# Performance work log

Measured on AMD Instinct MI355X. Metric: run time of the kernel, lower is better.

## Reference

```python
import jax, jax.numpy as jnp
import numpy as np

GRID_SIZE = 5
SPLINE_ORDER = 3
GRID_RANGE = (-0.2, 0.2)
N_TOK, IN_CH, OUT_CH = 8192, 1024, 1024
K_COEF = GRID_SIZE + SPLINE_ORDER  # 8 basis functions per feature


def _make_grid():
    lo, hi = GRID_RANGE
    h = (hi - lo) / GRID_SIZE
    # 12 knots, extended by spline_order on both sides
    return (jnp.arange(-SPLINE_ORDER, GRID_SIZE + SPLINE_ORDER + 1, dtype=jnp.float32) * h + lo)


def _b_splines(x, grid):
    # x: [N, in] -> bases: [N, in, K_COEF] via Cox-de Boor recursion
    xe = x[..., None]                      # [N, in, 1]
    G = grid.shape[0]                      # 12
    bases = ((xe >= grid[:-1]) & (xe < grid[1:])).astype(x.dtype)  # [N, in, G-1]
    for k in range(1, SPLINE_ORDER + 1):
        left = (xe - grid[: G - k - 1]) / (grid[k : G - 1] - grid[: G - k - 1]) * bases[..., :-1]
        right = (grid[k + 1 :] - xe) / (grid[k + 1 :] - grid[1 : G - k]) * bases[..., 1:]
        bases = left + right
    return bases                            # [N, in, 8]


def _kan_layer(x, base_w, spline_w, grid):
    # base_activation = Identity
    base_out = x @ base_w.T                               # [N, out]
    bases = _b_splines(x, grid)                           # [N, in, K]
    spline_out = jnp.einsum('nik,oik->no', bases, spline_w)
    return base_out + spline_out


def setup_inputs() -> dict:
    key = jax.random.key(0)
    k1, k2, k3, k4, k5 = jax.random.split(key, 5)
    lo, hi = GRID_RANGE
    x = jax.random.uniform(k1, (N_TOK, IN_CH), dtype=jnp.float32, minval=lo, maxval=hi)
    s = 0.1 / np.sqrt(IN_CH)
    return {
        'x': x,
        'base_w1': jax.random.normal(k2, (OUT_CH, IN_CH), dtype=jnp.float32) * s,
        'spline_w1': jax.random.normal(k3, (OUT_CH, IN_CH, K_COEF), dtype=jnp.float32) * s,
        'base_w2': jax.random.normal(k4, (OUT_CH, OUT_CH), dtype=jnp.float32) * s,
        'spline_w2': jax.random.normal(k5, (OUT_CH, OUT_CH, K_COEF), dtype=jnp.float32) * s,
    }


def reference(x, base_w1, spline_w1, base_w2, spline_w2):
    grid = _make_grid()
    x1 = _kan_layer(x, base_w1, spline_w1, grid)
    x2 = _kan_layer(x1, base_w2, spline_w2, grid)
    return x2
```

## Files before the change

### kernel.cpp

```cpp
#include <hip/hip_runtime.h>
#include <hip/hip_bf16.h>

typedef __attribute__((ext_vector_type(8))) short bf16x8;
typedef __attribute__((ext_vector_type(4))) float f32x4;
typedef __attribute__((ext_vector_type(4))) unsigned int u32x4;

#define KCAT 9216
#define NTOK 8192
#define CH   1024
#define KHALF 4608
#define NT32 144

__device__ __forceinline__ unsigned short f2bf(float f) {
    union { float f; unsigned int u; } v; v.f = f;
    unsigned int r = v.u + 0x7fffu + ((v.u >> 16) & 1u);
    return (unsigned short)(r >> 16);
}

__device__ __forceinline__ void load16_to_lds(const void* gp, void* lp) {
    __builtin_amdgcn_global_load_lds(
        (__attribute__((address_space(1))) void*)(void*)gp,
        (__attribute__((address_space(3))) void*)lp,
        16, 0, 0);
}

__device__ __forceinline__ void bases8_cf(float x, unsigned int* w) {
    float p  = (x + 0.44f) * 12.5f;
    float mf = floorf(p);
    float u  = p - mf;
    int   m  = (int)mf;
    float v  = 1.0f - u;
    float u2 = u * u, u3 = u2 * u;
    float N0 = v * v * v * (1.0f / 6.0f);
    float N1 = 0.5f * u3 - u2 + (2.0f / 3.0f);
    float N3 = u3 * (1.0f / 6.0f);
    float N2 = 1.0f - N0 - N1 - N3;
    unsigned long long lo =
          (unsigned long long)f2bf(N0)
        | ((unsigned long long)f2bf(N1) << 16)
        | ((unsigned long long)f2bf(N2) << 32)
        | ((unsigned long long)f2bf(N3) << 48);
    lo = (m >= 0 && m <= 10) ? lo : 0ull;
    int sh  = (m - 3) * 16;
    int sh1 = sh - 64;
    unsigned long long d0 =
        (sh  >= 0) ? ((sh  < 64) ? (lo << sh)    : 0ull)
                   : ((-sh  < 64) ? (lo >> (-sh))  : 0ull);
    unsigned long long d1 =
        (sh1 >= 0) ? ((sh1 < 64) ? (lo << sh1)   : 0ull)
                   : ((-sh1 < 64) ? (lo >> (-sh1)) : 0ull);
    w[0] = (unsigned int)d0; w[1] = (unsigned int)(d0 >> 32);
    w[2] = (unsigned int)d1; w[3] = (unsigned int)(d1 >> 32);
}

__device__ __forceinline__ void conv_w_body(const float* __restrict__ BW,
                                            const float* __restrict__ SW,
                                            unsigned short* __restrict__ W, int o) {
    const float* bw = BW + (size_t)o * 1024;
    const float* sw = SW + (size_t)o * 8192;
    unsigned short* w = W + (size_t)o * KCAT;
    for (int c = threadIdx.x * 4; c < KCAT; c += 256 * 4) {
        const float* src = (c < 1024) ? (bw + c) : (sw + (c - 1024));
        float4 v = *(const float4*)src;
        unsigned short u[4] = { f2bf(v.x), f2bf(v.y), f2bf(v.z), f2bf(v.w) };
        *(unsigned long long*)(w + c) = *(unsigned long long*)u;
    }
}

__device__ __forceinline__ void basis_body(float x, unsigned short* __restrict__ A, int idx) {
    int n = idx >> 10, i = idx & 1023;
    size_t rowbase = (size_t)n * KCAT;
    A[rowbase + i] = f2bf(x);
    unsigned int w[4];
    bases8_cf(x, w);
    *(u32x4*)(A + rowbase + 1024 + (size_t)i * 8) = (u32x4){w[0], w[1], w[2], w[3]};
}

__global__ __launch_bounds__(256) void prep1(const float* __restrict__ BW1,
                                             const float* __restrict__ SW1,
                                             unsigned short* __restrict__ W,
                                             const float* __restrict__ X,
                                             unsigned short* __restrict__ A) {
    int b = blockIdx.x;
    if (b < 1024) { conv_w_body(BW1, SW1, W, b); return; }
    int bb = b - 1024;
    for (int idx = bb * 256 + threadIdx.x; idx < NTOK * CH; idx += 2048 * 256)
        basis_body(X[idx], A, idx);
}

__global__ __launch_bounds__(256) void mid2(const float* __restrict__ BW2,
                                            const float* __restrict__ SW2,
                                            unsigned short* __restrict__ W,
                                            const float* __restrict__ C0,
                                            const float* __restrict__ C1,
                                            unsigned short* __restrict__ A) {
    int b = blockIdx.x;
    if (b < 1024) { conv_w_body(BW2, SW2, W, b); return; }
    int bb = b - 1024;
    for (int idx = bb * 256 + threadIdx.x; idx < NTOK * CH; idx += 2048 * 256)
        basis_body(C0[idx] + C1[idx], A, idx);
}

__global__ __launch_bounds__(256) void add_out(const float* __restrict__ C0,
                                               const float* __restrict__ C1,
                                               float* __restrict__ out, int total4) {
    for (int i = blockIdx.x * 256 + threadIdx.x; i < total4; i += gridDim.x * 256) {
        float4 a = ((const float4*)C0)[i];
        float4 b = ((const float4*)C1)[i];
        float4 r = { a.x + b.x, a.y + b.y, a.z + b.z, a.w + b.w };
        ((float4*)out)[i] = r;
    }
}

__global__ __launch_bounds__(512, 2) void gemm256_splitk(const unsigned short* __restrict__ A,
                                                         const unsigned short* __restrict__ B,
                                                         float* __restrict__ C0,
                                                         float* __restrict__ C1) {
    __shared__ __align__(16) unsigned short As[4 * 256 * 32];
    __shared__ __align__(16) unsigned short Bs[4 * 256 * 32];
    const int tid  = threadIdx.x;
    const int lane = tid & 63;
    const int wid  = tid >> 6;
    const int wr = wid >> 2, wc = wid & 3;
    const int ln = lane & 15, q = lane >> 4;

    const int bid = blockIdx.x;
    const int xcd = bid & 7, ii = bid >> 3;
    const int kz = xcd & 1, chm = xcd >> 1;
    const int bm = chm * 8 + (ii & 7);
    const int bn = ii >> 3;

    const unsigned short* Ab = A + (size_t)(bm * 256) * KCAT + (size_t)kz * KHALF;
    const unsigned short* Bb = B + (size_t)(bn * 256) * KCAT + (size_t)kz * KHALF;
    float* C = (kz == 0) ? C0 : C1;

    f32x4 acc[8][4] = {};

    auto stage = [&](int tile, int ds) {
#pragma unroll
        for (int part = 0; part < 2; ++part) {
            int c = part * 512 + tid;
            int r = c >> 2;
            int gslot = (c & 3) ^ ((r >> 1) & 3);
            size_t goff = (size_t)r * (KCAT * 2) + (size_t)tile * 64 + gslot * 16;
            load16_to_lds((const char*)Ab + goff, (char*)As + (size_t)ds * 16384 + c * 16);
            load16_to_lds((const char*)Bb + goff, (char*)Bs + (size_t)ds * 16384 + c * 16);
        }
    };

    stage(0, 0);
    stage(1, 1);
    asm volatile("s_waitcnt vmcnt(4)" ::: "memory");
    __builtin_amdgcn_s_barrier();

    for (int g = 0; g < NT32 / 4; ++g) {
#pragma unroll
        for (int u = 0; u < 4; ++u) {
            const int tile = g * 4 + u;
            const bool pf = (tile + 2) < NT32;
            if (pf) stage(tile + 2, (u + 2) & 3);

            const char* Ah = (const char*)As + u * 16384;
            const char* Bh = (const char*)Bs + u * 16384;
            bf16x8 afr[8], bfr[4];
#pragma unroll
            for (int f = 0; f < 8; ++f) {
                int row = wr * 128 + f * 16 + ln;
                afr[f] = *(const bf16x8*)(Ah + row * 64 + ((q ^ ((row >> 1) & 3)) * 16));
            }
#pragma unroll
            for (int nf = 0; nf < 4; ++nf) {
                int row = wc * 64 + nf * 16 + ln;
                bfr[nf] = *(const bf16x8*)(Bh + row * 64 + ((q ^ ((row >> 1) & 3)) * 16));
            }
            __builtin_amdgcn_s_setprio(1);
#pragma unroll
            for (int f = 0; f < 8; ++f)
#pragma unroll
                for (int nf = 0; nf < 4; ++nf)
                    acc[f][nf] = __builtin_amdgcn_mfma_f32_16x16x32_bf16(
                        afr[f], bfr[nf], acc[f][nf], 0, 0, 0);
            __builtin_amdgcn_s_setprio(0);
            if (pf) asm volatile("s_waitcnt vmcnt(4)" ::: "memory");
            else    asm volatile("s_waitcnt vmcnt(0)" ::: "memory");
            __builtin_amdgcn_s_barrier();
        }
    }

#pragma unroll
    for (int mf = 0; mf < 8; ++mf)
#pragma unroll
        for (int nf = 0; nf < 4; ++nf)
#pragma unroll
            for (int r = 0; r < 4; ++r) {
                int row = bm * 256 + wr * 128 + mf * 16 + q * 4 + r;
                int col = bn * 256 + wc * 64 + nf * 16 + ln;
                C[(size_t)row * CH + col] = acc[mf][nf][r];
            }
}

extern "C" void kernel_launch(void* const* d_in, const int* in_sizes, int n_in,
                              void* d_out, int out_size, void* d_ws, size_t ws_size,
                              hipStream_t stream) {
    const float* x   = (const float*)d_in[0];
    const float* bw1 = (const float*)d_in[1];
    const float* sw1 = (const float*)d_in[2];
    const float* bw2 = (const float*)d_in[3];
    const float* sw2 = (const float*)d_in[4];
    float* out = (float*)d_out;

    char* ws = (char*)d_ws;
    unsigned short* Abuf = (unsigned short*)ws;
    unsigned short* Wbuf = (unsigned short*)(ws + 150994944);
    float* C0 = (float*)(ws + 150994944 + 18874368);
    float* C1 = (float*)(ws + 150994944 + 18874368 + 33554432);

    prep1         <<<dim3(3072), dim3(256), 0, stream>>>(bw1, sw1, Wbuf, x, Abuf);
    gemm256_splitk<<<dim3(256), dim3(512), 0, stream>>>(Abuf, Wbuf, C0, C1);

    mid2          <<<dim3(3072), dim3(256), 0, stream>>>(bw2, sw2, Wbuf, C0, C1, Abuf);
    gemm256_splitk<<<dim3(256), dim3(512), 0, stream>>>(Abuf, Wbuf, C0, C1);
    add_out       <<<dim3(1024), dim3(256), 0, stream>>>(C0, C1, out, NTOK * CH / 4);
}
```

Measured before the change: 488.8 us.

## Switch to 32x32x16 MFMA and load B fragments directly into registers

Replaces the 16x16x32 bf16 MFMA tiling with 32x32x16 instructions. It removes the LDS staging of the B operand, so each wave loads its B fragments straight from global memory into double-buffered registers, one tile ahead of use. The goal is to cut LDS traffic and halve shared memory use while keeping the A tile in the existing four-stage LDS pipeline. The trade-off is uncoalesced, wave-duplicated global loads of B (four waves share each column slice), more register pressure, and a hand-unrolled tail with adjusted vmcnt waits.

```diff
diff --git a/kernel.cpp b/kernel.cpp
--- a/kernel.cpp
+++ b/kernel.cpp
@@ -2,7 +2,7 @@
 #include <hip/hip_bf16.h>
 
 typedef __attribute__((ext_vector_type(8))) short bf16x8;
-typedef __attribute__((ext_vector_type(4))) float f32x4;
+typedef __attribute__((ext_vector_type(16))) float f32x16;
 typedef __attribute__((ext_vector_type(4))) unsigned int u32x4;
 
 #define KCAT 9216
@@ -117,12 +117,11 @@
                                                          float* __restrict__ C0,
                                                          float* __restrict__ C1) {
     __shared__ __align__(16) unsigned short As[4 * 256 * 32];
-    __shared__ __align__(16) unsigned short Bs[4 * 256 * 32];
     const int tid  = threadIdx.x;
     const int lane = tid & 63;
     const int wid  = tid >> 6;
     const int wr = wid >> 2, wc = wid & 3;
-    const int ln = lane & 15, q = lane >> 4;
+    const int l31 = lane & 31, h = lane >> 5;
 
     const int bid = blockIdx.x;
     const int xcd = bid & 7, ii = bid >> 3;
@@ -131,12 +130,14 @@
     const int bn = ii >> 3;
 
     const unsigned short* Ab = A + (size_t)(bm * 256) * KCAT + (size_t)kz * KHALF;
-    const unsigned short* Bb = B + (size_t)(bn * 256) * KCAT + (size_t)kz * KHALF;
+    const unsigned short* Bl = B + (size_t)(bn * 256 + wc * 64 + l31) * KCAT
+                                 + (size_t)kz * KHALF + (size_t)h * 8;
     float* C = (kz == 0) ? C0 : C1;
 
-    f32x4 acc[8][4] = {};
-
-    auto stage = [&](int tile, int ds) {
+    f32x16 acc[4][2] = {};
+    bf16x8 b0[2][2], b1[2][2];
+
+    auto stageA = [&](int tile, int ds) {
 #pragma unroll
         for (int part = 0; part < 2; ++part) {
             int c = part * 512 + tid;
@@ -144,57 +145,72 @@
             int gslot = (c & 3) ^ ((r >> 1) & 3);
             size_t goff = (size_t)r * (KCAT * 2) + (size_t)tile * 64 + gslot * 16;
             load16_to_lds((const char*)Ab + goff, (char*)As + (size_t)ds * 16384 + c * 16);
-            load16_to_lds((const char*)Bb + goff, (char*)Bs + (size_t)ds * 16384 + c * 16);
         }
     };
-
-    stage(0, 0);
-    stage(1, 1);
-    asm volatile("s_waitcnt vmcnt(4)" ::: "memory");
+    auto loadB = [&](bf16x8 (&dst)[2][2], int tile) {
+#pragma unroll
+        for (int nf = 0; nf < 2; ++nf)
+#pragma unroll
+            for (int ks = 0; ks < 2; ++ks)
+                dst[nf][ks] = *(const bf16x8*)(Bl + (size_t)nf * 32 * KCAT
+                                                  + (size_t)tile * 32 + ks * 16);
+    };
+    auto compute = [&](const bf16x8 (&bfr)[2][2], int u) {
+        const char* Ah = (const char*)As + u * 16384;
+        bf16x8 afr[8];
+#pragma unroll
+        for (int mf = 0; mf < 4; ++mf)
+#pragma unroll
+            for (int ks = 0; ks < 2; ++ks) {
+                int row = wr * 128 + mf * 32 + l31;
+                int kslot = ks * 2 + h;
+                afr[mf * 2 + ks] = *(const bf16x8*)(Ah + row * 64
+                                      + ((kslot ^ ((row >> 1) & 3)) * 16));
+            }
+        __builtin_amdgcn_s_setprio(1);
+#pragma unroll
+        for (int ks = 0; ks < 2; ++ks)
+#pragma unroll
+            for (int mf = 0; mf < 4; ++mf)
+#pragma unroll
+                for (int nf = 0; nf < 2; ++nf)
+                    acc[mf][nf] = __builtin_amdgcn_mfma_f32_32x32x16_bf16(
+                        afr[mf * 2 + ks], bfr[nf][ks], acc[mf][nf], 0, 0, 0);
+        __builtin_amdgcn_s_setprio(0);
+    };
+
+    loadB(b0, 0);
+    stageA(0, 0);
+    stageA(1, 1);
+    asm volatile("s_waitcnt vmcnt(2)" ::: "memory");
     __builtin_amdgcn_s_barrier();
 
-    for (int g = 0; g < NT32 / 4; ++g) {
+    for (int g = 0; g < 35; ++g) {
+        const int t = g * 4;
 #pragma unroll
         for (int u = 0; u < 4; ++u) {
-            const int tile = g * 4 + u;
-            const bool pf = (tile + 2) < NT32;
-            if (pf) stage(tile + 2, (u + 2) & 3);
-
-            const char* Ah = (const char*)As + u * 16384;
-            const char* Bh = (const char*)Bs + u * 16384;
-            bf16x8 afr[8], bfr[4];
-#pragma unroll
-            for (int f = 0; f < 8; ++f) {
-                int row = wr * 128 + f * 16 + ln;
-                afr[f] = *(const bf16x8*)(Ah + row * 64 + ((q ^ ((row >> 1) & 3)) * 16));
-            }
-#pragma unroll
-            for (int nf = 0; nf < 4; ++nf) {
-                int row = wc * 64 + nf * 16 + ln;
-                bfr[nf] = *(const bf16x8*)(Bh + row * 64 + ((q ^ ((row >> 1) & 3)) * 16));
-            }
-            __builtin_amdgcn_s_setprio(1);
-#pragma unroll
-            for (int f = 0; f < 8; ++f)
-#pragma unroll
-                for (int nf = 0; nf < 4; ++nf)
-                    acc[f][nf] = __builtin_amdgcn_mfma_f32_16x16x32_bf16(
-                        afr[f], bfr[nf], acc[f][nf], 0, 0, 0);
-            __builtin_amdgcn_s_setprio(0);
-            if (pf) asm volatile("s_waitcnt vmcnt(4)" ::: "memory");
-            else    asm volatile("s_waitcnt vmcnt(0)" ::: "memory");
+            if ((u & 1) == 0) { loadB(b1, t + u + 1); stageA(t + u + 2, (u + 2) & 3); compute(b0, u); }
+            else              { loadB(b0, t + u + 1); stageA(t + u + 2, (u + 2) & 3); compute(b1, u); }
+            asm volatile("s_waitcnt vmcnt(6)" ::: "memory");
             __builtin_amdgcn_s_barrier();
         }
     }
-
-#pragma unroll
-    for (int mf = 0; mf < 8; ++mf)
-#pragma unroll
-        for (int nf = 0; nf < 4; ++nf)
-#pragma unroll
-            for (int r = 0; r < 4; ++r) {
-                int row = bm * 256 + wr * 128 + mf * 16 + q * 4 + r;
-                int col = bn * 256 + wc * 64 + nf * 16 + ln;
+    { loadB(b1, 141); stageA(142, 2); compute(b0, 0);
+      asm volatile("s_waitcnt vmcnt(6)" ::: "memory"); __builtin_amdgcn_s_barrier(); }
+    { loadB(b0, 142); stageA(143, 3); compute(b1, 1);
+      asm volatile("s_waitcnt vmcnt(6)" ::: "memory"); __builtin_amdgcn_s_barrier(); }
+    { loadB(b1, 143); compute(b0, 2);
+      asm volatile("s_waitcnt vmcnt(4)" ::: "memory"); __builtin_amdgcn_s_barrier(); }
+    { compute(b1, 3); }
+
+#pragma unroll
+    for (int mf = 0; mf < 4; ++mf)
+#pragma unroll
+        for (int nf = 0; nf < 2; ++nf)
+#pragma unroll
+            for (int r = 0; r < 16; ++r) {
+                int row = bm * 256 + wr * 128 + mf * 32 + (r & 3) + 8 * (r >> 2) + 4 * h;
+                int col = bn * 256 + wc * 64 + nf * 32 + l31;
                 C[(size_t)row * CH + col] = acc[mf][nf][r];
             }
 }
```

Result: slower. 615.3 us (+25.9%).
